# Performance work log

Hardware: AMD Instinct MI355X
Metric: run time of the kernel (lower is better)

The kernel has to match this reference:

```python
import jax, jax.numpy as jnp
import numpy as np

H, FFN, E, TOPK = 1024, 4096, 8, 2
B, S = 2, 1024


def setup_inputs() -> dict:
    key = jax.random.key(0)
    k1, k2, k3, k4 = jax.random.split(key, 4)
    s_h = 1.0 / np.sqrt(H).astype(np.float32)
    s_f = 1.0 / np.sqrt(FFN).astype(np.float32)
    return {
        "hidden_states": jax.random.normal(k1, (B, S, H), jnp.float32),
        "gate_w": jax.random.normal(k2, (E, H), jnp.float32) * s_h,       # router Linear(H->E), no bias
        "w13": jax.random.normal(k3, (E, 2 * FFN, H), jnp.float32) * s_h,  # fused [w1; w3] per expert
        "w2": jax.random.normal(k4, (E, H, FFN), jnp.float32) * s_f,       # down-proj per expert
        "top_k": TOPK,
    }


def reference(hidden_states, gate_w, w13, w2, top_k):
    b, s, h = hidden_states.shape
    x = hidden_states.reshape(-1, h)                       # [T, H]
    router_logits = x @ gate_w.T                           # [T, E]
    rw = jax.nn.softmax(router_logits.astype(jnp.float32), axis=1)
    rw, sel = jax.lax.top_k(rw, top_k)                     # [T, K] each
    rw = rw / rw.sum(axis=-1, keepdims=True)
    rw = rw.astype(x.dtype)
    e_tot = gate_w.shape[0]
    f = w2.shape[2]
    # combine[t, e] = sum_k rw[t, k] * (sel[t, k] == e)
    combine = jnp.sum((sel[..., None] == jnp.arange(e_tot)) * rw[..., None], axis=1)  # [T, E]
    out = jnp.zeros_like(x)
    for e in range(e_tot):  # static small loop over experts
        g = x @ w13[e, :f].T            # [T, F] gate proj
        u = x @ w13[e, f:].T            # [T, F] up proj
        y = (jax.nn.silu(g) * u) @ w2[e].T  # [T, H]
        out = out + combine[:, e:e + 1] * y
    return out.reshape(b, s, h), router_logits
```

## Files before the change

kernel.cpp:

```cpp
#include <hip/hip_runtime.h>
#include <hip/hip_bf16.h>
#include <math.h>

#define H     1024
#define FFN   4096
#define NE    8
#define TOK   2048
#define PAIRS (TOK*2)
#define BM    128
#define BK    32
#define ROWCAP (PAIRS + NE*BM)
#define MAXTILES (ROWCAP/BM)

typedef unsigned short u16;
typedef __attribute__((ext_vector_type(8))) __bf16 bf16x8;
typedef __attribute__((ext_vector_type(4))) float  f32x4;

__device__ __forceinline__ unsigned cvt2(float a, float b) {
    __hip_bfloat162 h = __float22bfloat162_rn(float2{a, b});
    unsigned u;
    __builtin_memcpy(&u, &h, 4);
    return u;
}

#define GLD16(gp, lp) __builtin_amdgcn_global_load_lds( \
    (const __attribute__((address_space(1))) void*)(gp), \
    (__attribute__((address_space(3))) void*)(lp), 16, 0, 0)

__global__ void k_init(int* counts) {
    if (threadIdx.x < NE) counts[threadIdx.x] = 0;
}

__global__ void k_router(const float* __restrict__ x, const float* __restrict__ gw,
                         float* __restrict__ logits, int* counts,
                         int* __restrict__ sel, int* __restrict__ posn, float* __restrict__ wgt) {
    int lane = threadIdx.x & 63;
    int t = blockIdx.x * 4 + (threadIdx.x >> 6);
    float p[NE];
#pragma unroll
    for (int e = 0; e < NE; e++) p[e] = 0.f;
    for (int j = 0; j < H / 64; j++) {
        int h = lane + j * 64;
        float xv = x[(size_t)t * H + h];
#pragma unroll
        for (int e = 0; e < NE; e++) p[e] = fmaf(xv, gw[e * H + h], p[e]);
    }
#pragma unroll
    for (int off = 32; off; off >>= 1)
#pragma unroll
        for (int e = 0; e < NE; e++) p[e] += __shfl_xor(p[e], off, 64);
    if (lane == 0) {
        float mx = p[0];
#pragma unroll
        for (int e = 1; e < NE; e++) mx = fmaxf(mx, p[e]);
        float pe[NE];
#pragma unroll
        for (int e = 0; e < NE; e++) pe[e] = __expf(p[e] - mx);
        int i0 = 0;
#pragma unroll
        for (int e = 1; e < NE; e++) if (pe[e] > pe[i0]) i0 = e;
        int i1 = (i0 == 0) ? 1 : 0;
#pragma unroll
        for (int e = 0; e < NE; e++) if (e != i1 && e != i0 && pe[e] > pe[i1]) i1 = e;
        float w0 = pe[i0] / (pe[i0] + pe[i1]);
#pragma unroll
        for (int e = 0; e < NE; e++) logits[(size_t)t * NE + e] = p[e];
        int p0 = atomicAdd(&counts[i0], 1);
        int p1 = atomicAdd(&counts[i1], 1);
        sel[2 * t] = i0;  posn[2 * t] = p0;  wgt[2 * t] = w0;
        sel[2 * t + 1] = i1;  posn[2 * t + 1] = p1;  wgt[2 * t + 1] = 1.f - w0;
    }
}

__global__ void k_prefix(const int* __restrict__ counts, int* __restrict__ base,
                         int* __restrict__ tile_e) {
    if (threadIdx.x == 0) {
        int b = 0, tb = 0;
        for (int e = 0; e < NE; e++) {
            base[e] = b;
            int nt = (counts[e] + BM - 1) / BM;
            for (int i = 0; i < nt; i++) tile_e[tb++] = e;
            b += nt * BM;
        }
        base[NE] = b;
        while (tb < MAXTILES) tile_e[tb++] = -1;
    }
}

__global__ void k_gather(const float4* __restrict__ x4, const int* __restrict__ sel,
                         const int* __restrict__ posn, const int* __restrict__ base,
                         u16* __restrict__ xg) {
    int p = blockIdx.x;
    int lane = threadIdx.x;
    int t = p >> 1;
    int row = base[sel[p]] + posn[p];
#pragma unroll
    for (int i = 0; i < 4; i++) {
        int idx = i * 64 + lane;
        float4 v = x4[(size_t)t * (H / 4) + idx];
        uint2 o = { cvt2(v.x, v.y), cvt2(v.z, v.w) };
        *(uint2*)&xg[(size_t)row * H + idx * 4] = o;
    }
}

__global__ __launch_bounds__(256) void k_gemm1(const u16* __restrict__ xg,
                                               const float* __restrict__ w13,
                                               u16* __restrict__ act,
                                               const int* __restrict__ tile_e) {
    int e = tile_e[blockIdx.x];
    if (e < 0) return;
    __shared__ u16 As[BM * BK];
    __shared__ u16 Bs[2][64 * (BK + 8)];

    int tid = threadIdx.x;
    int lane = tid & 63, wave = tid >> 6;
    int quad = lane >> 4, m16 = lane & 15;
    int wm = wave >> 1, wn = wave & 1;
    int row0 = blockIdx.x * BM;
    int n0 = blockIdx.y * 64;
    const float* wb1 = w13 + ((size_t)e * 2 * FFN + n0) * H;
    const float* wb3 = w13 + ((size_t)e * 2 * FFN + FFN + n0) * H;

    f32x4 accg[4][2], accu[4][2];
#pragma unroll
    for (int mi = 0; mi < 4; mi++)
#pragma unroll
        for (int ni = 0; ni < 2; ni++) { accg[mi][ni] = {0.f,0.f,0.f,0.f}; accu[mi][ni] = {0.f,0.f,0.f,0.f}; }

    for (int kk = 0; kk < H; kk += BK) {
#pragma unroll
        for (int i = 0; i < 2; i++) {
            int chunk = i * 256 + tid;
            int r = chunk >> 2, c = (chunk & 3) * 8;
            GLD16(xg + (size_t)(row0 + r) * H + kk + c, As + chunk * 8);
        }
#pragma unroll
        for (int i = 0; i < 2; i++) {
            int idx = i * 256 + tid;
            int r = idx >> 3, c4 = idx & 7;
            float4 v1 = *(const float4*)(wb1 + (size_t)r * H + kk + c4 * 4);
            float4 v3 = *(const float4*)(wb3 + (size_t)r * H + kk + c4 * 4);
            uint2 o1 = { cvt2(v1.x, v1.y), cvt2(v1.z, v1.w) };
            uint2 o3 = { cvt2(v3.x, v3.y), cvt2(v3.z, v3.w) };
            *(uint2*)&Bs[0][r * (BK + 8) + c4 * 4] = o1;
            *(uint2*)&Bs[1][r * (BK + 8) + c4 * 4] = o3;
        }
        __syncthreads();
        bf16x8 a[4], bg[2], bu[2];
#pragma unroll
        for (int mi = 0; mi < 4; mi++)
            a[mi] = *(const bf16x8*)&As[(wm * 64 + mi * 16 + m16) * BK + quad * 8];
#pragma unroll
        for (int ni = 0; ni < 2; ni++) {
            bg[ni] = *(const bf16x8*)&Bs[0][(wn * 32 + ni * 16 + m16) * (BK + 8) + quad * 8];
            bu[ni] = *(const bf16x8*)&Bs[1][(wn * 32 + ni * 16 + m16) * (BK + 8) + quad * 8];
        }
#pragma unroll
        for (int mi = 0; mi < 4; mi++)
#pragma unroll
            for (int ni = 0; ni < 2; ni++) {
                accg[mi][ni] = __builtin_amdgcn_mfma_f32_16x16x32_bf16(a[mi], bg[ni], accg[mi][ni], 0, 0, 0);
                accu[mi][ni] = __builtin_amdgcn_mfma_f32_16x16x32_bf16(a[mi], bu[ni], accu[mi][ni], 0, 0, 0);
            }
        __syncthreads();
    }
#pragma unroll
    for (int mi = 0; mi < 4; mi++)
#pragma unroll
        for (int ni = 0; ni < 2; ni++) {
            int gcol = n0 + wn * 32 + ni * 16 + m16;
            int grow = row0 + wm * 64 + mi * 16 + quad * 4;
#pragma unroll
            for (int r = 0; r < 4; r++) {
                float g = accg[mi][ni][r], u = accu[mi][ni][r];
                float hv = g * (1.f / (1.f + __expf(-g))) * u;
                unsigned pk = cvt2(hv, hv);
                act[(size_t)(grow + r) * FFN + gcol] = (u16)(pk & 0xffff);
            }
        }
}

__global__ __launch_bounds__(256) void k_gemm2(const u16* __restrict__ act,
                                               const float* __restrict__ w2,
                                               float* __restrict__ yc,
                                               const int* __restrict__ tile_e) {
    int e = tile_e[blockIdx.x];
    if (e < 0) return;
    __shared__ u16 As[BM * BK];
    __shared__ u16 Bs[BM * (BK + 8)];

    int tid = threadIdx.x;
    int lane = tid & 63, wave = tid >> 6;
    int quad = lane >> 4, m16 = lane & 15;
    int wm = wave >> 1, wn = wave & 1;
    int row0 = blockIdx.x * BM;
    int n0 = blockIdx.y * 128;
    int k0 = blockIdx.z * (FFN / 2);
    const float* wb = w2 + ((size_t)e * H + n0) * FFN;
    float* ycp = yc + (size_t)blockIdx.z * ROWCAP * H;

    f32x4 acc[4][4];
#pragma unroll
    for (int mi = 0; mi < 4; mi++)
#pragma unroll
        for (int ni = 0; ni < 4; ni++) acc[mi][ni] = {0.f,0.f,0.f,0.f};

    for (int kk = k0; kk < k0 + FFN / 2; kk += BK) {
#pragma unroll
        for (int i = 0; i < 2; i++) {
            int chunk = i * 256 + tid;
            int r = chunk >> 2, c = (chunk & 3) * 8;
            GLD16(act + (size_t)(row0 + r) * FFN + kk + c, As + chunk * 8);
        }
#pragma unroll
        for (int i = 0; i < 4; i++) {
            int idx = i * 256 + tid;
            int r = idx >> 3, c4 = idx & 7;
            float4 v = *(const float4*)(wb + (size_t)r * FFN + kk + c4 * 4);
            uint2 o = { cvt2(v.x, v.y), cvt2(v.z, v.w) };
            *(uint2*)&Bs[r * (BK + 8) + c4 * 4] = o;
        }
        __syncthreads();
        bf16x8 a[4], b[4];
#pragma unroll
        for (int mi = 0; mi < 4; mi++)
            a[mi] = *(const bf16x8*)&As[(wm * 64 + mi * 16 + m16) * BK + quad * 8];
#pragma unroll
        for (int ni = 0; ni < 4; ni++)
            b[ni] = *(const bf16x8*)&Bs[(wn * 64 + ni * 16 + m16) * (BK + 8) + quad * 8];
#pragma unroll
        for (int mi = 0; mi < 4; mi++)
#pragma unroll
            for (int ni = 0; ni < 4; ni++)
                acc[mi][ni] = __builtin_amdgcn_mfma_f32_16x16x32_bf16(a[mi], b[ni], acc[mi][ni], 0, 0, 0);
        __syncthreads();
    }
#pragma unroll
    for (int mi = 0; mi < 4; mi++)
#pragma unroll
        for (int ni = 0; ni < 4; ni++)
#pragma unroll
            for (int r = 0; r < 4; r++) {
                int grow = row0 + wm * 64 + mi * 16 + quad * 4 + r;
                int gcol = n0 + wn * 64 + ni * 16 + m16;
                ycp[(size_t)grow * H + gcol] = acc[mi][ni][r];
            }
}

__global__ void k_combine(const float4* __restrict__ yc4, const int* __restrict__ sel,
                          const int* __restrict__ posn, const int* __restrict__ base,
                          const float* __restrict__ wgt, float4* __restrict__ out4) {
    int t = blockIdx.x;
    int j = threadIdx.x;
    int r0 = base[sel[2 * t]] + posn[2 * t];
    int r1 = base[sel[2 * t + 1]] + posn[2 * t + 1];
    float w0 = wgt[2 * t], w1 = wgt[2 * t + 1];
    const size_t P = (size_t)ROWCAP * (H / 4);
    float4 a0 = yc4[(size_t)r0 * (H / 4) + j];
    float4 a1 = yc4[(size_t)r0 * (H / 4) + j + P];
    float4 b0 = yc4[(size_t)r1 * (H / 4) + j];
    float4 b1 = yc4[(size_t)r1 * (H / 4) + j + P];
    float4 o = { w0 * (a0.x + a1.x) + w1 * (b0.x + b1.x),
                 w0 * (a0.y + a1.y) + w1 * (b0.y + b1.y),
                 w0 * (a0.z + a1.z) + w1 * (b0.z + b1.z),
                 w0 * (a0.w + a1.w) + w1 * (b0.w + b1.w) };
    out4[(size_t)t * (H / 4) + j] = o;
}

extern "C" void kernel_launch(void* const* d_in, const int* in_sizes, int n_in,
                              void* d_out, int out_size, void* d_ws, size_t ws_size,
                              hipStream_t stream) {
    const float* x   = (const float*)d_in[0];
    const float* gw  = (const float*)d_in[1];
    const float* w13 = (const float*)d_in[2];
    const float* w2  = (const float*)d_in[3];
    float* out    = (float*)d_out;
    float* logits = out + (size_t)TOK * H;

    char* ws = (char*)d_ws;
    int*   counts = (int*)ws;
    int*   base   = (int*)(ws + 256);
    int*   tile_e = (int*)(ws + 512);
    int*   sel    = (int*)(ws + 1024);
    int*   posn   = (int*)(ws + 1024 + 4 * PAIRS);
    float* wgt    = (float*)(ws + 1024 + 8 * PAIRS);
    u16*   xg     = (u16*)(ws + 65536);
    u16*   act    = xg + (size_t)ROWCAP * H;
    float* yc     = (float*)(act + (size_t)ROWCAP * FFN);

    k_init<<<1, 64, 0, stream>>>(counts);
    k_router<<<TOK / 4, 256, 0, stream>>>(x, gw, logits, counts, sel, posn, wgt);
    k_prefix<<<1, 64, 0, stream>>>(counts, base, tile_e);
    k_gather<<<PAIRS, 64, 0, stream>>>((const float4*)x, sel, posn, base, xg);
    dim3 g1(MAXTILES, FFN / 64);
    k_gemm1<<<g1, 256, 0, stream>>>(xg, w13, act, tile_e);
    dim3 g2(MAXTILES, H / 128, 2);
    k_gemm2<<<g2, 256, 0, stream>>>(act, w2, yc, tile_e);
    k_combine<<<TOK, 256, 0, stream>>>((const float4*)yc, sel, posn, base, wgt, (float4*)out);
}
```

Baseline: 718.6 us.

## Double-buffer GEMM LDS tiles, swizzle A layout, and remap blocks per XCD

Both expert GEMM kernels now use double-buffered shared memory. The next K-slice (A via global_load_lds, B via register prefetch then convert) is loaded while MFMAs run on the current slice, which leaves one barrier per iteration. The gathered x rows and activation columns are written in an XOR-swizzled order so the unpadded A tile reads avoid LDS bank conflicts. The 2D/3D grids are flattened and remapped so blocks sharing the same weight column slab land on the same XCD for better L2 reuse. The cost is doubled LDS and more registers, which may lower occupancy.

```diff
diff --git a/kernel.cpp b/kernel.cpp
--- a/kernel.cpp
+++ b/kernel.cpp
@@ -27,6 +27,7 @@
     (const __attribute__((address_space(1))) void*)(gp), \
     (__attribute__((address_space(3))) void*)(lp), 16, 0, 0)
 
+
 __global__ void k_init(int* counts) {
     if (threadIdx.x < NE) counts[threadIdx.x] = 0;
 }
@@ -94,10 +95,11 @@
     int lane = threadIdx.x;
     int t = p >> 1;
     int row = base[sel[p]] + posn[p];
+    int f2 = ((row >> 1) & 3) << 1;
 #pragma unroll
     for (int i = 0; i < 4; i++) {
         int idx = i * 64 + lane;
-        float4 v = x4[(size_t)t * (H / 4) + idx];
+        float4 v = x4[(size_t)t * (H / 4) + (idx ^ f2)];
         uint2 o = { cvt2(v.x, v.y), cvt2(v.z, v.w) };
         *(uint2*)&xg[(size_t)row * H + idx * 4] = o;
     }
@@ -107,17 +109,22 @@
                                                const float* __restrict__ w13,
                                                u16* __restrict__ act,
                                                const int* __restrict__ tile_e) {
-    int e = tile_e[blockIdx.x];
+    int id = blockIdx.x;
+    int xcd = id & 7;
+    int j = id >> 3;
+    int tile = j % MAXTILES;
+    int n0i = xcd * 8 + j / MAXTILES;
+    int e = tile_e[tile];
     if (e < 0) return;
-    __shared__ u16 As[BM * BK];
-    __shared__ u16 Bs[2][64 * (BK + 8)];
+    __shared__ u16 As[2][BM * BK];
+    __shared__ u16 Bs[2][2][64 * (BK + 8)];
 
     int tid = threadIdx.x;
     int lane = tid & 63, wave = tid >> 6;
     int quad = lane >> 4, m16 = lane & 15;
     int wm = wave >> 1, wn = wave & 1;
-    int row0 = blockIdx.x * BM;
-    int n0 = blockIdx.y * 64;
+    int row0 = tile * BM;
+    int n0 = n0i * 64;
     const float* wb1 = w13 + ((size_t)e * 2 * FFN + n0) * H;
     const float* wb3 = w13 + ((size_t)e * 2 * FFN + FFN + n0) * H;
 
@@ -127,33 +134,55 @@
 #pragma unroll
         for (int ni = 0; ni < 2; ni++) { accg[mi][ni] = {0.f,0.f,0.f,0.f}; accu[mi][ni] = {0.f,0.f,0.f,0.f}; }
 
-    for (int kk = 0; kk < H; kk += BK) {
-#pragma unroll
-        for (int i = 0; i < 2; i++) {
-            int chunk = i * 256 + tid;
-            int r = chunk >> 2, c = (chunk & 3) * 8;
-            GLD16(xg + (size_t)(row0 + r) * H + kk + c, As + chunk * 8);
-        }
-#pragma unroll
-        for (int i = 0; i < 2; i++) {
-            int idx = i * 256 + tid;
-            int r = idx >> 3, c4 = idx & 7;
-            float4 v1 = *(const float4*)(wb1 + (size_t)r * H + kk + c4 * 4);
-            float4 v3 = *(const float4*)(wb3 + (size_t)r * H + kk + c4 * 4);
-            uint2 o1 = { cvt2(v1.x, v1.y), cvt2(v1.z, v1.w) };
-            uint2 o3 = { cvt2(v3.x, v3.y), cvt2(v3.z, v3.w) };
-            *(uint2*)&Bs[0][r * (BK + 8) + c4 * 4] = o1;
-            *(uint2*)&Bs[1][r * (BK + 8) + c4 * 4] = o3;
-        }
-        __syncthreads();
+    float4 v1[2], v3[2];
+#pragma unroll
+    for (int i = 0; i < 2; i++) {
+        int chunk = i * 256 + tid;
+        GLD16(xg + (size_t)(row0 + (chunk >> 2)) * H + (chunk & 3) * 8, As[0] + chunk * 8);
+    }
+#pragma unroll
+    for (int i = 0; i < 2; i++) {
+        int idx = i * 256 + tid;
+        v1[i] = *(const float4*)(wb1 + (size_t)(idx >> 3) * H + (idx & 7) * 4);
+        v3[i] = *(const float4*)(wb3 + (size_t)(idx >> 3) * H + (idx & 7) * 4);
+    }
+#pragma unroll
+    for (int i = 0; i < 2; i++) {
+        int idx = i * 256 + tid;
+        int r = idx >> 3, c4 = idx & 7;
+        uint2 o1 = { cvt2(v1[i].x, v1[i].y), cvt2(v1[i].z, v1[i].w) };
+        uint2 o3 = { cvt2(v3[i].x, v3[i].y), cvt2(v3[i].z, v3[i].w) };
+        *(uint2*)&Bs[0][0][r * (BK + 8) + c4 * 4] = o1;
+        *(uint2*)&Bs[0][1][r * (BK + 8) + c4 * 4] = o3;
+    }
+    __syncthreads();
+
+    int aslot = quad ^ ((m16 >> 1) & 3);
+    for (int it = 0; it < H / BK; ++it) {
+        int cur = it & 1, nxt = cur ^ 1;
+        int kk = (it + 1) * BK;
+        bool pf = kk < H;
+        if (pf) {
+#pragma unroll
+            for (int i = 0; i < 2; i++) {
+                int chunk = i * 256 + tid;
+                GLD16(xg + (size_t)(row0 + (chunk >> 2)) * H + kk + (chunk & 3) * 8, As[nxt] + chunk * 8);
+            }
+#pragma unroll
+            for (int i = 0; i < 2; i++) {
+                int idx = i * 256 + tid;
+                v1[i] = *(const float4*)(wb1 + (size_t)(idx >> 3) * H + kk + (idx & 7) * 4);
+                v3[i] = *(const float4*)(wb3 + (size_t)(idx >> 3) * H + kk + (idx & 7) * 4);
+            }
+        }
         bf16x8 a[4], bg[2], bu[2];
 #pragma unroll
         for (int mi = 0; mi < 4; mi++)
-            a[mi] = *(const bf16x8*)&As[(wm * 64 + mi * 16 + m16) * BK + quad * 8];
+            a[mi] = *(const bf16x8*)&As[cur][(wm * 64 + mi * 16 + m16) * BK + aslot * 8];
 #pragma unroll
         for (int ni = 0; ni < 2; ni++) {
-            bg[ni] = *(const bf16x8*)&Bs[0][(wn * 32 + ni * 16 + m16) * (BK + 8) + quad * 8];
-            bu[ni] = *(const bf16x8*)&Bs[1][(wn * 32 + ni * 16 + m16) * (BK + 8) + quad * 8];
+            bg[ni] = *(const bf16x8*)&Bs[cur][0][(wn * 32 + ni * 16 + m16) * (BK + 8) + quad * 8];
+            bu[ni] = *(const bf16x8*)&Bs[cur][1][(wn * 32 + ni * 16 + m16) * (BK + 8) + quad * 8];
         }
 #pragma unroll
         for (int mi = 0; mi < 4; mi++)
@@ -162,6 +191,18 @@
                 accg[mi][ni] = __builtin_amdgcn_mfma_f32_16x16x32_bf16(a[mi], bg[ni], accg[mi][ni], 0, 0, 0);
                 accu[mi][ni] = __builtin_amdgcn_mfma_f32_16x16x32_bf16(a[mi], bu[ni], accu[mi][ni], 0, 0, 0);
             }
+        __builtin_amdgcn_sched_barrier(0);
+        if (pf) {
+#pragma unroll
+            for (int i = 0; i < 2; i++) {
+                int idx = i * 256 + tid;
+                int r = idx >> 3, c4 = idx & 7;
+                uint2 o1 = { cvt2(v1[i].x, v1[i].y), cvt2(v1[i].z, v1[i].w) };
+                uint2 o3 = { cvt2(v3[i].x, v3[i].y), cvt2(v3[i].z, v3[i].w) };
+                *(uint2*)&Bs[nxt][0][r * (BK + 8) + c4 * 4] = o1;
+                *(uint2*)&Bs[nxt][1][r * (BK + 8) + c4 * 4] = o3;
+            }
+        }
         __syncthreads();
     }
 #pragma unroll
@@ -174,8 +215,8 @@
             for (int r = 0; r < 4; r++) {
                 float g = accg[mi][ni][r], u = accu[mi][ni][r];
                 float hv = g * (1.f / (1.f + __expf(-g))) * u;
-                unsigned pk = cvt2(hv, hv);
-                act[(size_t)(grow + r) * FFN + gcol] = (u16)(pk & 0xffff);
+                int f = ((quad * 4 + r) >> 1) & 3;
+                act[(size_t)(grow + r) * FFN + (gcol ^ (f << 3))] = (u16)(cvt2(hv, hv) & 0xffff);
             }
         }
 }
@@ -184,20 +225,26 @@
                                                const float* __restrict__ w2,
                                                float* __restrict__ yc,
                                                const int* __restrict__ tile_e) {
-    int e = tile_e[blockIdx.x];
+    int id = blockIdx.x;
+    int xcd = id & 7;
+    int j = id >> 3;
+    int tile = j % MAXTILES;
+    int pz = xcd * 2 + j / MAXTILES;
+    int e = tile_e[tile];
     if (e < 0) return;
-    __shared__ u16 As[BM * BK];
-    __shared__ u16 Bs[BM * (BK + 8)];
+    __shared__ u16 As[2][BM * BK];
+    __shared__ u16 Bs[2][BM * (BK + 8)];
 
     int tid = threadIdx.x;
     int lane = tid & 63, wave = tid >> 6;
     int quad = lane >> 4, m16 = lane & 15;
     int wm = wave >> 1, wn = wave & 1;
-    int row0 = blockIdx.x * BM;
-    int n0 = blockIdx.y * 128;
-    int k0 = blockIdx.z * (FFN / 2);
+    int row0 = tile * BM;
+    int n0 = (pz >> 1) * 128;
+    int z = pz & 1;
+    int k0 = z * (FFN / 2);
     const float* wb = w2 + ((size_t)e * H + n0) * FFN;
-    float* ycp = yc + (size_t)blockIdx.z * ROWCAP * H;
+    float* ycp = yc + (size_t)z * ROWCAP * H;
 
     f32x4 acc[4][4];
 #pragma unroll
@@ -205,34 +252,66 @@
 #pragma unroll
         for (int ni = 0; ni < 4; ni++) acc[mi][ni] = {0.f,0.f,0.f,0.f};
 
-    for (int kk = k0; kk < k0 + FFN / 2; kk += BK) {
-#pragma unroll
-        for (int i = 0; i < 2; i++) {
-            int chunk = i * 256 + tid;
-            int r = chunk >> 2, c = (chunk & 3) * 8;
-            GLD16(act + (size_t)(row0 + r) * FFN + kk + c, As + chunk * 8);
-        }
-#pragma unroll
-        for (int i = 0; i < 4; i++) {
-            int idx = i * 256 + tid;
-            int r = idx >> 3, c4 = idx & 7;
-            float4 v = *(const float4*)(wb + (size_t)r * FFN + kk + c4 * 4);
-            uint2 o = { cvt2(v.x, v.y), cvt2(v.z, v.w) };
-            *(uint2*)&Bs[r * (BK + 8) + c4 * 4] = o;
-        }
-        __syncthreads();
+    float4 v[4];
+#pragma unroll
+    for (int i = 0; i < 2; i++) {
+        int chunk = i * 256 + tid;
+        GLD16(act + (size_t)(row0 + (chunk >> 2)) * FFN + k0 + (chunk & 3) * 8, As[0] + chunk * 8);
+    }
+#pragma unroll
+    for (int i = 0; i < 4; i++) {
+        int idx = i * 256 + tid;
+        v[i] = *(const float4*)(wb + (size_t)(idx >> 3) * FFN + k0 + (idx & 7) * 4);
+    }
+#pragma unroll
+    for (int i = 0; i < 4; i++) {
+        int idx = i * 256 + tid;
+        int r = idx >> 3, c4 = idx & 7;
+        uint2 o = { cvt2(v[i].x, v[i].y), cvt2(v[i].z, v[i].w) };
+        *(uint2*)&Bs[0][r * (BK + 8) + c4 * 4] = o;
+    }
+    __syncthreads();
+
+    int aslot = quad ^ ((m16 >> 1) & 3);
+    const int NT = (FFN / 2) / BK;
+    for (int it = 0; it < NT; ++it) {
+        int cur = it & 1, nxt = cur ^ 1;
+        int kk = k0 + (it + 1) * BK;
+        bool pf = (it + 1) < NT;
+        if (pf) {
+#pragma unroll
+            for (int i = 0; i < 2; i++) {
+                int chunk = i * 256 + tid;
+                GLD16(act + (size_t)(row0 + (chunk >> 2)) * FFN + kk + (chunk & 3) * 8, As[nxt] + chunk * 8);
+            }
+#pragma unroll
+            for (int i = 0; i < 4; i++) {
+                int idx = i * 256 + tid;
+                v[i] = *(const float4*)(wb + (size_t)(idx >> 3) * FFN + kk + (idx & 7) * 4);
+            }
+        }
         bf16x8 a[4], b[4];
 #pragma unroll
         for (int mi = 0; mi < 4; mi++)
-            a[mi] = *(const bf16x8*)&As[(wm * 64 + mi * 16 + m16) * BK + quad * 8];
+            a[mi] = *(const bf16x8*)&As[cur][(wm * 64 + mi * 16 + m16) * BK + aslot * 8];
 #pragma unroll
         for (int ni = 0; ni < 4; ni++)
-            b[ni] = *(const bf16x8*)&Bs[(wn * 64 + ni * 16 + m16) * (BK + 8) + quad * 8];
+            b[ni] = *(const bf16x8*)&Bs[cur][(wn * 64 + ni * 16 + m16) * (BK + 8) + quad * 8];
 #pragma unroll
         for (int mi = 0; mi < 4; mi++)
 #pragma unroll
             for (int ni = 0; ni < 4; ni++)
                 acc[mi][ni] = __builtin_amdgcn_mfma_f32_16x16x32_bf16(a[mi], b[ni], acc[mi][ni], 0, 0, 0);
+        __builtin_amdgcn_sched_barrier(0);
+        if (pf) {
+#pragma unroll
+            for (int i = 0; i < 4; i++) {
+                int idx = i * 256 + tid;
+                int r = idx >> 3, c4 = idx & 7;
+                uint2 o = { cvt2(v[i].x, v[i].y), cvt2(v[i].z, v[i].w) };
+                *(uint2*)&Bs[nxt][r * (BK + 8) + c4 * 4] = o;
+            }
+        }
         __syncthreads();
     }
 #pragma unroll
@@ -292,9 +371,7 @@
     k_router<<<TOK / 4, 256, 0, stream>>>(x, gw, logits, counts, sel, posn, wgt);
     k_prefix<<<1, 64, 0, stream>>>(counts, base, tile_e);
     k_gather<<<PAIRS, 64, 0, stream>>>((const float4*)x, sel, posn, base, xg);
-    dim3 g1(MAXTILES, FFN / 64);
-    k_gemm1<<<g1, 256, 0, stream>>>(xg, w13, act, tile_e);
-    dim3 g2(MAXTILES, H / 128, 2);
-    k_gemm2<<<g2, 256, 0, stream>>>(act, w2, yc, tile_e);
+    k_gemm1<<<dim3(MAXTILES * (FFN / 64)), 256, 0, stream>>>(xg, w13, act, tile_e);
+    k_gemm2<<<dim3(MAXTILES * (H / 128) * 2), 256, 0, stream>>>(act, w2, yc, tile_e);
     k_combine<<<TOK, 256, 0, stream>>>((const float4*)yc, sel, posn, base, wgt, (float4*)out);
 }
```

After: 683.4 us. 4.9% less time.
